# Performance work log

Measured on AMD Instinct MI355X. Metric: run time of the kernel, lower is better.

Reference implementation:

```python
import jax, jax.numpy as jnp
import numpy as np

B, S, DIM, H = 2, 2048, 1024, 16
DH = DIM // H


def setup_inputs() -> dict:
    key = jax.random.key(0)
    ks = jax.random.split(key, 12)
    sd = 0.02
    inp = {
        "query": jax.random.normal(ks[0], (B, S, DIM), jnp.float32),
        "key": jax.random.normal(ks[1], (B, S, DIM), jnp.float32),
        "value": jax.random.normal(ks[2], (B, S, DIM), jnp.float32),
        "pad_mask": jax.random.randint(ks[3], (B, 1, 1, S), 0, 2, jnp.int32),
        "training_status": 1,
        "Wq": jax.random.normal(ks[4], (DIM, DIM), jnp.float32) * sd,
        "bq": jnp.zeros((DIM,), jnp.float32),
        "Wk": jax.random.normal(ks[5], (DIM, DIM), jnp.float32) * sd,
        "bk": jnp.zeros((DIM,), jnp.float32),
        "Wv": jax.random.normal(ks[6], (DIM, DIM), jnp.float32) * sd,
        "bv": jnp.zeros((DIM,), jnp.float32),
        "Wf": jax.random.normal(ks[7], (DIM, DIM), jnp.float32) * sd,
        "bf": jnp.zeros((DIM,), jnp.float32),
    }
    return inp


def reference(query, key, value, pad_mask, training_status, Wq, bq, Wk, bk, Wv, bv, Wf, bf):
    b, s, _ = query.shape
    # projections, split heads -> [B, H, S, Dh]
    def split_heads(x):
        return x.reshape(b, -1, H, DH).transpose(0, 2, 1, 3)

    q = split_heads(query @ Wq + bq)
    k = split_heads(key @ Wk + bk)
    v = split_heads(value @ Wv + bv)

    # NOTE: original divides by sqrt(Dh) twice (explicit + self.scale) => /Dh
    scores = jnp.einsum("bhqd,bhkd->bhqk", q, k) / jnp.asarray(DH, q.dtype)
    if training_status:
        scores = jnp.where(pad_mask == 0, jnp.asarray(-1e9, scores.dtype), scores)
    attn = jax.nn.softmax(scores, axis=-1)
    out = jnp.einsum("bhqk,bhkd->bhqd", attn, v)  # [B,H,S,Dh]
    out = out.transpose(0, 2, 1, 3).reshape(b, s, DIM)
    return out @ Wf + bf
```

## Files before the change

kernel.cpp:

```cpp
#include <hip/hip_runtime.h>

#define Bn   2
#define Sn   2048
#define DIMn 1024
#define Hn   16
#define DHn  64

typedef unsigned short u16;
typedef unsigned int   u32;

typedef __attribute__((ext_vector_type(8))) __bf16 bf16x8;
typedef __attribute__((ext_vector_type(8))) float  f32x8v;
typedef __attribute__((ext_vector_type(4))) float  f32x4;

__device__ __forceinline__ u16 f2bf(float f) {
    union { float f; u32 u; } v; v.f = f;
    u32 r = v.u + 0x7fffu + ((v.u >> 16) & 1u);
    return (u16)(r >> 16);
}
__device__ __forceinline__ bf16x8 ldfrag(const u16* p) {
    union { uint4 u; bf16x8 v; } x;
    x.u = *(const uint4*)p;
    return x.v;
}
__device__ __forceinline__ uint4 pack8(const u16 h[8]) {
    uint4 r;
    r.x = (u32)h[0] | ((u32)h[1] << 16);
    r.y = (u32)h[2] | ((u32)h[3] << 16);
    r.z = (u32)h[4] | ((u32)h[5] << 16);
    r.w = (u32)h[6] | ((u32)h[7] << 16);
    return r;
}
__device__ __forceinline__ void gl_lds16(const void* g, void* l) {
    __builtin_amdgcn_global_load_lds(
        (const __attribute__((address_space(1))) void*)g,
        (__attribute__((address_space(3))) void*)l, 16, 0, 0);
}

__global__ __launch_bounds__(256) void prep_weights(
    const float* __restrict__ Wq, const float* __restrict__ Wk,
    const float* __restrict__ Wv, const float* __restrict__ Wf,
    u16* __restrict__ Wt)
{
    __shared__ __align__(16) float tile[64][68];
    const float* W = (blockIdx.z == 0) ? Wq : (blockIdx.z == 1) ? Wk
                   : (blockIdx.z == 2) ? Wv : Wf;
    u16* out = Wt + (size_t)blockIdx.z * DIMn * DIMn;
    const int t = threadIdx.x;
    const int n0 = blockIdx.x * 64, k0 = blockIdx.y * 64;
    const int rr = t >> 4, cc = (t & 15) * 4;
#pragma unroll
    for (int i = 0; i < 4; i++)
        *(float4*)&tile[rr + 16 * i][cc] =
            *(const float4*)(W + (size_t)(k0 + rr + 16 * i) * DIMn + n0 + cc);
    __syncthreads();
#pragma unroll
    for (int e = 0; e < 2; e++) {
        const int ci = 2 * t + e;
        const int n = ci >> 3, kc = ci & 7;
        u16 h[8];
#pragma unroll
        for (int j = 0; j < 8; j++) h[j] = f2bf(tile[kc * 8 + j][n]);
        *(uint4*)(out + (size_t)(n0 + n) * DIMn + k0 + kc * 8) = pack8(h);
    }
}

__global__ __launch_bounds__(256) void gemm_qkv(
    const float* __restrict__ Aq, const float* __restrict__ Ak,
    const float* __restrict__ Av, const u16* __restrict__ Wt,
    const float* __restrict__ bqp, const float* __restrict__ bkp,
    const float* __restrict__ bvp, u16* __restrict__ Qw,
    u16* __restrict__ Kw, u16* __restrict__ VwT)
{
    __shared__ union {
        struct { __align__(16) float Afp[64 * 64];
                 __align__(16) u16   Bbf[32 * 128]; } s;
        __align__(16) u16 Ep[32][144];
    } L;

    const int f = blockIdx.x;
    const int xcd = f & 7;
    const int q = f >> 3;
    const int z = q >> 5;
    const int rem = q & 31;
    const int yi = rem >> 3, x = rem & 7;
    const int y = xcd * 4 + yi;
    const int m0 = y * 128, n0 = x * 128;

    const float* A    = (z == 0) ? Aq  : (z == 1) ? Ak  : Av;
    const float* bias = (z == 0) ? bqp : (z == 1) ? bkp : bvp;
    const u16* Bt = Wt + (size_t)z * DIMn * DIMn;

    const int t = threadIdx.x;
    const int lane = t & 63, wave = t >> 6;
    const int quad = lane >> 4, l15 = lane & 15;
    const int wm = wave >> 1, wn = wave & 1;

    const float* baseA[4];
#pragma unroll
    for (int s = 0; s < 4; s++) {
        const int c = wave * 16 + s * 4 + (lane >> 4);
        const int g = c >> 3, qq = (c >> 1) & 3, h = c & 1;
        baseA[s] = A + (size_t)(m0 + g * 16 + l15) * DIMn + qq * 8 + h * 4;
    }
    const u16* baseB[2];
#pragma unroll
    for (int s = 0; s < 2; s++) {
        const int c = wave * 8 + s * 4 + (lane >> 4);
        const int jg = c >> 2, qq = c & 3;
        baseB[s] = Bt + (size_t)(n0 + jg * 16 + l15) * DIMn + qq * 8;
    }

    f32x4 acc[4][4];
#pragma unroll
    for (int i = 0; i < 4; i++)
#pragma unroll
        for (int j = 0; j < 4; j++) acc[i][j] = (f32x4){0.f, 0.f, 0.f, 0.f};

    for (int k0 = 0; k0 < DIMn; k0 += 32) {
        __syncthreads();
#pragma unroll
        for (int s = 0; s < 4; s++)
            gl_lds16(baseA[s] + k0, &L.s.Afp[(wave * 16 + s * 4) * 64]);
#pragma unroll
        for (int s = 0; s < 2; s++)
            gl_lds16(baseB[s] + k0, &L.s.Bbf[(wave * 8 + s * 4) * 128]);
        __syncthreads();

        bf16x8 a[4], b[4];
#pragma unroll
        for (int i = 0; i < 4; i++) {
            const int g = wm * 4 + i;
            union { struct { f32x4 lo, hi; } p; f32x8v v; } u;
            u.p.lo = *(const f32x4*)&L.s.Afp[(g * 8 + quad * 2 + 0) * 64 + l15 * 4];
            u.p.hi = *(const f32x4*)&L.s.Afp[(g * 8 + quad * 2 + 1) * 64 + l15 * 4];
            a[i] = __builtin_convertvector(u.v, bf16x8);
        }
#pragma unroll
        for (int j = 0; j < 4; j++)
            b[j] = ldfrag(&L.s.Bbf[((wn * 4 + j) * 4 + quad) * 128 + l15 * 8]);
#pragma unroll
        for (int i = 0; i < 4; i++)
#pragma unroll
            for (int j = 0; j < 4; j++)
                acc[i][j] = __builtin_amdgcn_mfma_f32_16x16x32_bf16(a[i], b[j], acc[i][j], 0, 0, 0);
    }

    float bv[4];
#pragma unroll
    for (int j = 0; j < 4; j++) bv[j] = bias[n0 + wn * 64 + j * 16 + l15];

    const int bb = y >> 4;

    if (z < 2) {
        u16* out = (z == 0) ? Qw : Kw;
#pragma unroll
        for (int i = 0; i < 4; i++) {
            __syncthreads();
#pragma unroll
            for (int j = 0; j < 4; j++)
#pragma unroll
                for (int r = 0; r < 4; r++)
                    L.Ep[wm * 16 + quad * 4 + r][wn * 64 + j * 16 + l15] =
                        f2bf(acc[i][j][r] + bv[j]);
            __syncthreads();
#pragma unroll
            for (int e = 0; e < 2; e++) {
                const int ci = t + 256 * e;
                const int row = ci >> 4, c = ci & 15;
                const uint4 v = *(const uint4*)&L.Ep[row][c * 8];
                const int m = m0 + (row >> 4) * 64 + i * 16 + (row & 15);
                const int ss = m & 2047;
                const int n = n0 + c * 8;
                const int hh = n >> 6, dd = n & 63;
                *(uint4*)(out + ((size_t)(bb * Hn + hh) * Sn + ss) * DHn + dd) = v;
            }
        }
    } else {
#pragma unroll
        for (int j = 0; j < 4; j++) {
            __syncthreads();
#pragma unroll
            for (int i = 0; i < 4; i++) {
                u16 h4[4];
#pragma unroll
                for (int r = 0; r < 4; r++) h4[r] = f2bf(acc[i][j][r] + bv[j]);
                uint2 pk;
                pk.x = (u32)h4[0] | ((u32)h4[1] << 16);
                pk.y = (u32)h4[2] | ((u32)h4[3] << 16);
                *(uint2*)&L.Ep[wn * 16 + l15][wm * 64 + i * 16 + quad * 4] = pk;
            }
            __syncthreads();
#pragma unroll
            for (int e = 0; e < 2; e++) {
                const int ci = t + 256 * e;
                const int row = ci >> 4, c = ci & 15;
                const uint4 v = *(const uint4*)&L.Ep[row][c * 8];
                const int n = n0 + (row >> 4) * 64 + j * 16 + (row & 15);
                const int hh = n >> 6, dd = n & 63;
                const int ss = (m0 & 2047) + c * 8;
                *(uint4*)(VwT + ((size_t)(bb * Hn + hh) * DHn + dd) * Sn + ss) = v;
            }
        }
    }
}

__global__ __launch_bounds__(256) void gemm_final(
    const u16* __restrict__ A, const u16* __restrict__ Bt,
    const float* __restrict__ bias, float* __restrict__ out)
{
    __shared__ __align__(16) u16 Abf[32 * 128];
    __shared__ __align__(16) u16 Bbf[32 * 128];

    const int f = blockIdx.x;
    const int xcd = f & 7, q = f >> 3;
    const int y = xcd * 4 + (q >> 3), x = q & 7;
    const int m0 = y * 128, n0 = x * 128;

    const int t = threadIdx.x;
    const int lane = t & 63, wave = t >> 6;
    const int quad = lane >> 4, l15 = lane & 15;
    const int wm = wave >> 1, wn = wave & 1;

    int arow[2], aq[2];
#pragma unroll
    for (int s = 0; s < 2; s++) {
        const int c = wave * 8 + s * 4 + (lane >> 4);
        arow[s] = (c >> 2) * 16 + l15;
        aq[s] = c & 3;
    }
    const u16* baseB[2];
#pragma unroll
    for (int s = 0; s < 2; s++) {
        const int c = wave * 8 + s * 4 + (lane >> 4);
        baseB[s] = Bt + (size_t)(n0 + (c >> 2) * 16 + l15) * DIMn + (c & 3) * 8;
    }

    f32x4 acc[4][4];
#pragma unroll
    for (int i = 0; i < 4; i++)
#pragma unroll
        for (int j = 0; j < 4; j++) acc[i][j] = (f32x4){0.f, 0.f, 0.f, 0.f};

    for (int k0 = 0; k0 < DIMn; k0 += 32) {
        const int hh = k0 >> 6, d64 = k0 & 63;
        __syncthreads();
#pragma unroll
        for (int s = 0; s < 2; s++) {
            const int m = m0 + arow[s], bb = m >> 11, ss = m & 2047;
            const u16* gp = A + ((size_t)(bb * Hn + hh) * Sn + ss) * DHn + d64 + aq[s] * 8;
            gl_lds16(gp, &Abf[(wave * 8 + s * 4) * 128]);
        }
#pragma unroll
        for (int s = 0; s < 2; s++)
            gl_lds16(baseB[s] + k0, &Bbf[(wave * 8 + s * 4) * 128]);
        __syncthreads();

        bf16x8 a[4], b[4];
#pragma unroll
        for (int i = 0; i < 4; i++)
            a[i] = ldfrag(&Abf[((wm * 4 + i) * 4 + quad) * 128 + l15 * 8]);
#pragma unroll
        for (int j = 0; j < 4; j++)
            b[j] = ldfrag(&Bbf[((wn * 4 + j) * 4 + quad) * 128 + l15 * 8]);
#pragma unroll
        for (int i = 0; i < 4; i++)
#pragma unroll
            for (int j = 0; j < 4; j++)
                acc[i][j] = __builtin_amdgcn_mfma_f32_16x16x32_bf16(a[i], b[j], acc[i][j], 0, 0, 0);
    }

    float bv[4];
#pragma unroll
    for (int j = 0; j < 4; j++) bv[j] = bias[n0 + wn * 64 + j * 16 + l15];

#pragma unroll
    for (int i = 0; i < 4; i++)
#pragma unroll
        for (int j = 0; j < 4; j++) {
            const int n = n0 + wn * 64 + j * 16 + l15;
#pragma unroll
            for (int r = 0; r < 4; r++) {
                const int m = m0 + wm * 64 + i * 16 + quad * 4 + r;
                out[(size_t)m * DIMn + n] = acc[i][j][r] + bv[j];
            }
        }
}

__global__ __launch_bounds__(256) void attn_mfma(
    const u16* __restrict__ Qw, const u16* __restrict__ Kw,
    const u16* __restrict__ VwT, const int* __restrict__ mask,
    const int* __restrict__ tstat, u16* __restrict__ Aw)
{
    __shared__ __align__(16) u16 Kbf[32 * 128];
    __shared__ __align__(16) u16 Vbf[32 * 128];
    __shared__ __align__(16) u16 Ps[64][72];
    __shared__ int Msk[64];

    const int f = blockIdx.x;
    const int xcd = f & 7, q = f >> 3;
    const int p = xcd * 4 + (q >> 5);
    const int qt = q & 31;
    const int b = p >> 4, h = p & 15;
    const int q0 = qt * 64;

    const int t = threadIdx.x;
    const int lane = t & 63, wave = t >> 6;
    const int quad = lane >> 4, l15 = lane & 15;
    const bool use_mask = (tstat[0] != 0);
    const size_t slab = (size_t)(b * Hn + h) * Sn * DHn;

    const u16* baseK[2];
    const u16* baseV[2];
#pragma unroll
    for (int s = 0; s < 2; s++) {
        const int c = wave * 8 + s * 4 + (lane >> 4);
        const int rg = c >> 3, qp = c & 7;
        baseK[s] = Kw  + slab + (size_t)(rg * 16 + l15) * DHn + qp * 8;
        baseV[s] = VwT + slab + (size_t)(rg * 16 + l15) * Sn  + qp * 8;
    }

    bf16x8 aq[2];
#pragma unroll
    for (int ks = 0; ks < 2; ks++) {
        union { uint4 u; bf16x8 v; } xx;
        xx.u = *(const uint4*)(Qw + slab + (size_t)(q0 + wave * 16 + l15) * DHn + ks * 32 + quad * 8);
        aq[ks] = xx.v;
    }

    float lsum[4] = {0.f, 0.f, 0.f, 0.f};
    f32x4 O[4];
#pragma unroll
    for (int dt = 0; dt < 4; dt++) O[dt] = (f32x4){0.f, 0.f, 0.f, 0.f};

    for (int j0 = 0; j0 < Sn; j0 += 64) {
        __syncthreads();
#pragma unroll
        for (int s = 0; s < 2; s++) {
            gl_lds16(baseK[s] + (size_t)j0 * DHn, &Kbf[(wave * 8 + s * 4) * 128]);
            gl_lds16(baseV[s] + j0,               &Vbf[(wave * 8 + s * 4) * 128]);
        }
        if (t < 64) Msk[t] = use_mask ? mask[b * Sn + j0 + t] : 1;
        __syncthreads();

        f32x4 s[4];
#pragma unroll
        for (int ct = 0; ct < 4; ct++) s[ct] = (f32x4){0.f, 0.f, 0.f, 0.f};
#pragma unroll
        for (int ct = 0; ct < 4; ct++)
#pragma unroll
            for (int ks = 0; ks < 2; ks++) {
                const bf16x8 bk = ldfrag(&Kbf[(ct * 8 + ks * 4 + quad) * 128 + l15 * 8]);
                s[ct] = __builtin_amdgcn_mfma_f32_16x16x32_bf16(aq[ks], bk, s[ct], 0, 0, 0);
            }

        int mc[4];
#pragma unroll
        for (int ct = 0; ct < 4; ct++) mc[ct] = Msk[ct * 16 + l15];
#pragma unroll
        for (int ct = 0; ct < 4; ct++)
#pragma unroll
            for (int r = 0; r < 4; r++) {
                const float sv = mc[ct] ? s[ct][r] * (1.0f / 64.0f) : -1e9f;
                const float pp = __expf(sv);
                lsum[r] += pp;
                Ps[wave * 16 + quad * 4 + r][ct * 16 + l15] = f2bf(pp);
            }
        asm volatile("s_waitcnt lgkmcnt(0)" ::: "memory");

        bf16x8 pa[2];
#pragma unroll
        for (int kc = 0; kc < 2; kc++)
            pa[kc] = ldfrag(&Ps[wave * 16 + l15][kc * 32 + quad * 8]);
#pragma unroll
        for (int dt = 0; dt < 4; dt++)
#pragma unroll
            for (int kc = 0; kc < 2; kc++) {
                const bf16x8 bvv = ldfrag(&Vbf[(dt * 8 + kc * 4 + quad) * 128 + l15 * 8]);
                O[dt] = __builtin_amdgcn_mfma_f32_16x16x32_bf16(pa[kc], bvv, O[dt], 0, 0, 0);
            }
    }

#pragma unroll
    for (int r = 0; r < 4; r++) {
#pragma unroll
        for (int off = 1; off < 16; off <<= 1) lsum[r] += __shfl_xor(lsum[r], off);
    }

#pragma unroll
    for (int r = 0; r < 4; r++) {
        const float linv = 1.0f / fmaxf(lsum[r], 1e-30f);
        const int srow = q0 + wave * 16 + quad * 4 + r;
#pragma unroll
        for (int dt = 0; dt < 4; dt++)
            Aw[slab + (size_t)srow * DHn + dt * 16 + l15] = f2bf(O[dt][r] * linv);
    }
}

extern "C" void kernel_launch(void* const* d_in, const int* in_sizes, int n_in,
                              void* d_out, int out_size, void* d_ws, size_t ws_size,
                              hipStream_t stream) {
    const float* query = (const float*)d_in[0];
    const float* key   = (const float*)d_in[1];
    const float* value = (const float*)d_in[2];
    const int*   pmask = (const int*)d_in[3];
    const int*   tstat = (const int*)d_in[4];
    const float* Wq  = (const float*)d_in[5];
    const float* bq  = (const float*)d_in[6];
    const float* Wk  = (const float*)d_in[7];
    const float* bk  = (const float*)d_in[8];
    const float* Wv  = (const float*)d_in[9];
    const float* bv  = (const float*)d_in[10];
    const float* Wf  = (const float*)d_in[11];
    const float* bfb = (const float*)d_in[12];
    float* outp = (float*)d_out;

    const size_t NT = (size_t)Bn * Sn * DIMn;
    u16* Qw  = (u16*)d_ws;
    u16* Kw  = Qw + NT;
    u16* VwT = Kw + NT;
    u16* Wt  = VwT + NT;
    const size_t WSZ = (size_t)DIMn * DIMn;

    prep_weights<<<dim3(16, 16, 4), 256, 0, stream>>>(Wq, Wk, Wv, Wf, Wt);

    gemm_qkv<<<768, 256, 0, stream>>>(query, key, value, Wt, bq, bk, bv, Qw, Kw, VwT);

    attn_mfma<<<1024, 256, 0, stream>>>(Qw, Kw, VwT, pmask, tstat, Qw);

    gemm_final<<<256, 256, 0, stream>>>(Qw, Wt + 3 * WSZ, bfb, outp);
}
```

Measured before the change: 300.3 us.

## Multi-buffer LDS staging with async loads and bitmask pad mask

Double-buffers the QKV GEMM and attention kernels and triple-buffers the output GEMM. Global-to-LDS loads for upcoming k-tiles are issued ahead, using explicit vmcnt waits and raw s_barrier in place of full __syncthreads, so memory latency overlaps MFMA work. The attention kernel packs the pad mask into per-lane bit words once up front, dropping the per-tile mask load and barrier, and XOR-swizzles the P scratch tile to avoid LDS bank conflicts. The hand-counted vmcnt thresholds and larger LDS footprint add correctness risk and may lower occupancy.

```diff
diff --git a/kernel.cpp b/kernel.cpp
--- a/kernel.cpp
+++ b/kernel.cpp
@@ -35,6 +35,11 @@
     __builtin_amdgcn_global_load_lds(
         (const __attribute__((address_space(1))) void*)g,
         (__attribute__((address_space(3))) void*)l, 16, 0, 0);
+}
+__device__ __forceinline__ void barrier_nodrain() {
+    asm volatile("" ::: "memory");
+    __builtin_amdgcn_s_barrier();
+    asm volatile("" ::: "memory");
 }
 
 __global__ __launch_bounds__(256) void prep_weights(
@@ -73,8 +78,8 @@
     u16* __restrict__ Kw, u16* __restrict__ VwT)
 {
     __shared__ union {
-        struct { __align__(16) float Afp[64 * 64];
-                 __align__(16) u16   Bbf[32 * 128]; } s;
+        struct { __align__(16) float Afp[2][64 * 64];
+                 __align__(16) u16   Bbf[2][32 * 128]; } s;
         __align__(16) u16 Ep[32][144];
     } L;
 
@@ -99,51 +104,66 @@
     const float* baseA[4];
 #pragma unroll
     for (int s = 0; s < 4; s++) {
-        const int c = wave * 16 + s * 4 + (lane >> 4);
+        const int c = wave * 16 + s * 4 + quad;
         const int g = c >> 3, qq = (c >> 1) & 3, h = c & 1;
         baseA[s] = A + (size_t)(m0 + g * 16 + l15) * DIMn + qq * 8 + h * 4;
     }
     const u16* baseB[2];
 #pragma unroll
     for (int s = 0; s < 2; s++) {
-        const int c = wave * 8 + s * 4 + (lane >> 4);
+        const int c = wave * 8 + s * 4 + quad;
         const int jg = c >> 2, qq = c & 3;
         baseB[s] = Bt + (size_t)(n0 + jg * 16 + l15) * DIMn + qq * 8;
     }
 
+    auto STAGE = [&](int tt, int buf) {
+        const int k0 = tt * 32;
+#pragma unroll
+        for (int s = 0; s < 4; s++)
+            gl_lds16(baseA[s] + k0, &L.s.Afp[buf][(wave * 16 + s * 4) * 64]);
+#pragma unroll
+        for (int s = 0; s < 2; s++)
+            gl_lds16(baseB[s] + k0, &L.s.Bbf[buf][(wave * 8 + s * 4) * 128]);
+    };
+
     f32x4 acc[4][4];
 #pragma unroll
     for (int i = 0; i < 4; i++)
 #pragma unroll
         for (int j = 0; j < 4; j++) acc[i][j] = (f32x4){0.f, 0.f, 0.f, 0.f};
 
-    for (int k0 = 0; k0 < DIMn; k0 += 32) {
-        __syncthreads();
-#pragma unroll
-        for (int s = 0; s < 4; s++)
-            gl_lds16(baseA[s] + k0, &L.s.Afp[(wave * 16 + s * 4) * 64]);
-#pragma unroll
-        for (int s = 0; s < 2; s++)
-            gl_lds16(baseB[s] + k0, &L.s.Bbf[(wave * 8 + s * 4) * 128]);
-        __syncthreads();
+    const int NT = DIMn / 32;
+    STAGE(0, 0);
+    STAGE(1, 1);
+
+#pragma unroll 2
+    for (int tt = 0; tt < NT; ++tt) {
+        const int buf = tt & 1;
+        if (tt < NT - 1) asm volatile("s_waitcnt vmcnt(6)" ::: "memory");
+        else             asm volatile("s_waitcnt vmcnt(0)" ::: "memory");
+        barrier_nodrain();
 
         bf16x8 a[4], b[4];
 #pragma unroll
         for (int i = 0; i < 4; i++) {
             const int g = wm * 4 + i;
             union { struct { f32x4 lo, hi; } p; f32x8v v; } u;
-            u.p.lo = *(const f32x4*)&L.s.Afp[(g * 8 + quad * 2 + 0) * 64 + l15 * 4];
-            u.p.hi = *(const f32x4*)&L.s.Afp[(g * 8 + quad * 2 + 1) * 64 + l15 * 4];
+            u.p.lo = *(const f32x4*)&L.s.Afp[buf][(g * 8 + quad * 2 + 0) * 64 + l15 * 4];
+            u.p.hi = *(const f32x4*)&L.s.Afp[buf][(g * 8 + quad * 2 + 1) * 64 + l15 * 4];
             a[i] = __builtin_convertvector(u.v, bf16x8);
         }
 #pragma unroll
         for (int j = 0; j < 4; j++)
-            b[j] = ldfrag(&L.s.Bbf[((wn * 4 + j) * 4 + quad) * 128 + l15 * 8]);
+            b[j] = ldfrag(&L.s.Bbf[buf][((wn * 4 + j) * 4 + quad) * 128 + l15 * 8]);
 #pragma unroll
         for (int i = 0; i < 4; i++)
 #pragma unroll
             for (int j = 0; j < 4; j++)
                 acc[i][j] = __builtin_amdgcn_mfma_f32_16x16x32_bf16(a[i], b[j], acc[i][j], 0, 0, 0);
+
+        asm volatile("s_waitcnt lgkmcnt(0)" ::: "memory");
+        barrier_nodrain();
+        if (tt + 2 < NT) STAGE(tt + 2, buf);
     }
 
     float bv[4];
@@ -209,8 +229,8 @@
     const u16* __restrict__ A, const u16* __restrict__ Bt,
     const float* __restrict__ bias, float* __restrict__ out)
 {
-    __shared__ __align__(16) u16 Abf[32 * 128];
-    __shared__ __align__(16) u16 Bbf[32 * 128];
+    __shared__ __align__(16) u16 Abf[3][32 * 128];
+    __shared__ __align__(16) u16 Bbf[3][32 * 128];
 
     const int f = blockIdx.x;
     const int xcd = f & 7, q = f >> 3;
@@ -225,49 +245,65 @@
     int arow[2], aq[2];
 #pragma unroll
     for (int s = 0; s < 2; s++) {
-        const int c = wave * 8 + s * 4 + (lane >> 4);
+        const int c = wave * 8 + s * 4 + quad;
         arow[s] = (c >> 2) * 16 + l15;
         aq[s] = c & 3;
     }
     const u16* baseB[2];
 #pragma unroll
     for (int s = 0; s < 2; s++) {
-        const int c = wave * 8 + s * 4 + (lane >> 4);
+        const int c = wave * 8 + s * 4 + quad;
         baseB[s] = Bt + (size_t)(n0 + (c >> 2) * 16 + l15) * DIMn + (c & 3) * 8;
     }
 
-    f32x4 acc[4][4];
-#pragma unroll
-    for (int i = 0; i < 4; i++)
-#pragma unroll
-        for (int j = 0; j < 4; j++) acc[i][j] = (f32x4){0.f, 0.f, 0.f, 0.f};
-
-    for (int k0 = 0; k0 < DIMn; k0 += 32) {
-        const int hh = k0 >> 6, d64 = k0 & 63;
-        __syncthreads();
+    auto STAGE = [&](int tt, int buf) {
+        const int hh = tt >> 1, d64 = (tt & 1) * 32;
 #pragma unroll
         for (int s = 0; s < 2; s++) {
             const int m = m0 + arow[s], bb = m >> 11, ss = m & 2047;
             const u16* gp = A + ((size_t)(bb * Hn + hh) * Sn + ss) * DHn + d64 + aq[s] * 8;
-            gl_lds16(gp, &Abf[(wave * 8 + s * 4) * 128]);
+            gl_lds16(gp, &Abf[buf][(wave * 8 + s * 4) * 128]);
         }
 #pragma unroll
         for (int s = 0; s < 2; s++)
-            gl_lds16(baseB[s] + k0, &Bbf[(wave * 8 + s * 4) * 128]);
-        __syncthreads();
+            gl_lds16(baseB[s] + tt * 32, &Bbf[buf][(wave * 8 + s * 4) * 128]);
+    };
+
+    f32x4 acc[4][4];
+#pragma unroll
+    for (int i = 0; i < 4; i++)
+#pragma unroll
+        for (int j = 0; j < 4; j++) acc[i][j] = (f32x4){0.f, 0.f, 0.f, 0.f};
+
+    const int NT = DIMn / 32;
+    STAGE(0, 0);
+    STAGE(1, 1);
+    STAGE(2, 2);
+
+    int buf = 0;
+    for (int tt = 0; tt < NT; ++tt) {
+        if (tt < NT - 2)       asm volatile("s_waitcnt vmcnt(8)" ::: "memory");
+        else if (tt == NT - 2) asm volatile("s_waitcnt vmcnt(4)" ::: "memory");
+        else                   asm volatile("s_waitcnt vmcnt(0)" ::: "memory");
+        barrier_nodrain();
 
         bf16x8 a[4], b[4];
 #pragma unroll
         for (int i = 0; i < 4; i++)
-            a[i] = ldfrag(&Abf[((wm * 4 + i) * 4 + quad) * 128 + l15 * 8]);
+            a[i] = ldfrag(&Abf[buf][((wm * 4 + i) * 4 + quad) * 128 + l15 * 8]);
 #pragma unroll
         for (int j = 0; j < 4; j++)
-            b[j] = ldfrag(&Bbf[((wn * 4 + j) * 4 + quad) * 128 + l15 * 8]);
+            b[j] = ldfrag(&Bbf[buf][((wn * 4 + j) * 4 + quad) * 128 + l15 * 8]);
 #pragma unroll
         for (int i = 0; i < 4; i++)
 #pragma unroll
             for (int j = 0; j < 4; j++)
                 acc[i][j] = __builtin_amdgcn_mfma_f32_16x16x32_bf16(a[i], b[j], acc[i][j], 0, 0, 0);
+
+        asm volatile("s_waitcnt lgkmcnt(0)" ::: "memory");
+        barrier_nodrain();
+        if (tt + 3 < NT) STAGE(tt + 3, buf);
+        buf = (buf == 2) ? 0 : buf + 1;
     }
 
     float bv[4];
@@ -292,10 +328,9 @@
     const u16* __restrict__ VwT, const int* __restrict__ mask,
     const int* __restrict__ tstat, u16* __restrict__ Aw)
 {
-    __shared__ __align__(16) u16 Kbf[32 * 128];
-    __shared__ __align__(16) u16 Vbf[32 * 128];
-    __shared__ __align__(16) u16 Ps[64][72];
-    __shared__ int Msk[64];
+    __shared__ __align__(16) u16 Kbf[2][32 * 128];
+    __shared__ __align__(16) u16 Vbf[2][32 * 128];
+    __shared__ __align__(16) u16 Ps[64 * 64];
 
     const int f = blockIdx.x;
     const int xcd = f & 7, q = f >> 3;
@@ -314,12 +349,18 @@
     const u16* baseV[2];
 #pragma unroll
     for (int s = 0; s < 2; s++) {
-        const int c = wave * 8 + s * 4 + (lane >> 4);
+        const int c = wave * 8 + s * 4 + quad;
         const int rg = c >> 3, qp = c & 7;
         baseK[s] = Kw  + slab + (size_t)(rg * 16 + l15) * DHn + qp * 8;
         baseV[s] = VwT + slab + (size_t)(rg * 16 + l15) * Sn  + qp * 8;
     }
 
+    {
+        const int4* msrc4 = (const int4*)(mask + (size_t)b * Sn);
+        int4* mdst4 = (int4*)&Kbf[0][0];
+        mdst4[t]       = msrc4[t];
+        mdst4[t + 256] = msrc4[t + 256];
+    }
     bf16x8 aq[2];
 #pragma unroll
     for (int ks = 0; ks < 2; ks++) {
@@ -327,21 +368,46 @@
         xx.u = *(const uint4*)(Qw + slab + (size_t)(q0 + wave * 16 + l15) * DHn + ks * 32 + quad * 8);
         aq[ks] = xx.v;
     }
+    __syncthreads();
+
+    u32 mw0 = 0, mw1 = 0, mw2 = 0, mw3 = 0;
+    {
+        const int* ml = (const int*)&Kbf[0][0];
+#pragma unroll
+        for (int k = 0; k < 128; k++) {
+            const u32 bit = (ml[k * 16 + l15] != 0) ? 1u : 0u;
+            if (k < 32)      mw0 |= bit << k;
+            else if (k < 64) mw1 |= bit << (k - 32);
+            else if (k < 96) mw2 |= bit << (k - 64);
+            else             mw3 |= bit << (k - 96);
+        }
+    }
+    __syncthreads();
+
+    auto STAGE = [&](int tt, int buf) {
+        const int j0 = tt * 64;
+#pragma unroll
+        for (int s = 0; s < 2; s++) {
+            gl_lds16(baseK[s] + (size_t)j0 * DHn, &Kbf[buf][(wave * 8 + s * 4) * 128]);
+            gl_lds16(baseV[s] + j0,               &Vbf[buf][(wave * 8 + s * 4) * 128]);
+        }
+    };
 
     float lsum[4] = {0.f, 0.f, 0.f, 0.f};
     f32x4 O[4];
 #pragma unroll
     for (int dt = 0; dt < 4; dt++) O[dt] = (f32x4){0.f, 0.f, 0.f, 0.f};
 
-    for (int j0 = 0; j0 < Sn; j0 += 64) {
-        __syncthreads();
-#pragma unroll
-        for (int s = 0; s < 2; s++) {
-            gl_lds16(baseK[s] + (size_t)j0 * DHn, &Kbf[(wave * 8 + s * 4) * 128]);
-            gl_lds16(baseV[s] + j0,               &Vbf[(wave * 8 + s * 4) * 128]);
-        }
-        if (t < 64) Msk[t] = use_mask ? mask[b * Sn + j0 + t] : 1;
-        __syncthreads();
+    const int NT = Sn / 64;
+    STAGE(0, 0);
+    STAGE(1, 1);
+
+#pragma unroll 2
+    for (int tt = 0; tt < NT; ++tt) {
+        const int buf = tt & 1;
+        if (tt < NT - 1) asm volatile("s_waitcnt vmcnt(4)" ::: "memory");
+        else             asm volatile("s_waitcnt vmcnt(0)" ::: "memory");
+        barrier_nodrain();
 
         f32x4 s[4];
 #pragma unroll
@@ -350,13 +416,18 @@
         for (int ct = 0; ct < 4; ct++)
 #pragma unroll
             for (int ks = 0; ks < 2; ks++) {
-                const bf16x8 bk = ldfrag(&Kbf[(ct * 8 + ks * 4 + quad) * 128 + l15 * 8]);
+                const bf16x8 bk = ldfrag(&Kbf[buf][(ct * 8 + ks * 4 + quad) * 128 + l15 * 8]);
                 s[ct] = __builtin_amdgcn_mfma_f32_16x16x32_bf16(aq[ks], bk, s[ct], 0, 0, 0);
             }
 
-        int mc[4];
-#pragma unroll
-        for (int ct = 0; ct < 4; ct++) mc[ct] = Msk[ct * 16 + l15];
+        const int wsel = tt >> 3;
+        const u32 cw = (wsel == 0) ? mw0 : (wsel == 1) ? mw1 : (wsel == 2) ? mw2 : mw3;
+        const int sh = (tt & 7) * 4;
+        u32 mc[4];
+#pragma unroll
+        for (int ct = 0; ct < 4; ct++)
+            mc[ct] = use_mask ? ((cw >> (sh + ct)) & 1u) : 1u;
+
 #pragma unroll
         for (int ct = 0; ct < 4; ct++)
 #pragma unroll
@@ -364,21 +435,27 @@
                 const float sv = mc[ct] ? s[ct][r] * (1.0f / 64.0f) : -1e9f;
                 const float pp = __expf(sv);
                 lsum[r] += pp;
-                Ps[wave * 16 + quad * 4 + r][ct * 16 + l15] = f2bf(pp);
+                const int prow = wave * 16 + quad * 4 + r;
+                Ps[prow * 64 + ((ct * 16 + l15) ^ ((prow & 7) << 3))] = f2bf(pp);
             }
         asm volatile("s_waitcnt lgkmcnt(0)" ::: "memory");
 
         bf16x8 pa[2];
+        const int rrow = wave * 16 + l15;
 #pragma unroll
         for (int kc = 0; kc < 2; kc++)
-            pa[kc] = ldfrag(&Ps[wave * 16 + l15][kc * 32 + quad * 8]);
+            pa[kc] = ldfrag(&Ps[rrow * 64 + ((kc * 32 + quad * 8) ^ ((l15 & 7) << 3))]);
 #pragma unroll
         for (int dt = 0; dt < 4; dt++)
 #pragma unroll
             for (int kc = 0; kc < 2; kc++) {
-                const bf16x8 bvv = ldfrag(&Vbf[(dt * 8 + kc * 4 + quad) * 128 + l15 * 8]);
+                const bf16x8 bvv = ldfrag(&Vbf[buf][(dt * 8 + kc * 4 + quad) * 128 + l15 * 8]);
                 O[dt] = __builtin_amdgcn_mfma_f32_16x16x32_bf16(pa[kc], bvv, O[dt], 0, 0, 0);
             }
+
+        asm volatile("s_waitcnt lgkmcnt(0)" ::: "memory");
+        barrier_nodrain();
+        if (tt + 2 < NT) STAGE(tt + 2, buf);
     }
 
 #pragma unroll
```

Measured after the change: 307.6 us. 1.02x slower.
